# Kernel optimization log

Hardware: AMD Instinct MI355X
Metric: run time of the kernel (lower is better)

## Reference

```python
import jax, jax.numpy as jnp
import numpy as np

N = 4_194_304  # total observations
NBAND = 8      # photometric bands


def setup_inputs() -> dict:
    key = jax.random.key(0)
    ks = jax.random.split(key, 6)
    t = jnp.sort(jax.random.uniform(ks[0], (N,), dtype=jnp.float32) * 10000.0)
    band = jax.random.randint(ks[1], (N,), 0, NBAND)
    y = jax.random.normal(ks[2], (N,), dtype=jnp.float32) * 0.5
    diag = jax.random.uniform(ks[3], (N,), dtype=jnp.float32) * 0.1 + 0.01
    log_amp_delta = jax.random.normal(ks[4], (NBAND - 1,), dtype=jnp.float32) * 0.1
    lag = jax.random.uniform(ks[5], (NBAND - 1,), dtype=jnp.float32) * 5.0
    # exponential (DRW) celerite term: k(tau) = a * exp(-c * tau)
    log_kernel_param = jnp.array([0.0, -3.0], dtype=jnp.float32)
    return {"t": t, "band": band, "y": y, "diag": diag,
            "log_amp_delta": log_amp_delta, "lag": lag,
            "log_kernel_param": log_kernel_param}


def reference(t, band, y, diag, log_amp_delta, lag, log_kernel_param):
    # amp/lag transforms: prepend 0 for the reference band (jnp.insert at 0)
    log_amps = jnp.concatenate([jnp.zeros((1,), log_amp_delta.dtype), log_amp_delta])
    lags = jnp.concatenate([jnp.zeros((1,), lag.dtype), lag])

    # lag-shift times per band, then sort (GP requires sorted inputs)
    new_t = t - lags[band]
    inds = jnp.argsort(new_t)
    ts, bs, ys, ds = new_t[inds], band[inds], y[inds], diag[inds]

    # multiband kernel: K_ij = amp_i * amp_j * a * exp(-c * |t_i - t_j|) + diag_i * delta_ij
    amps = jnp.exp(log_amps)[bs]                 # [N]
    a = jnp.exp(log_kernel_param[0])
    c = jnp.exp(log_kernel_param[1])
    A = ds + a * amps * amps                     # diagonal of K
    U = a * amps                                 # low-rank left factor
    V = amps                                     # low-rank right factor
    dt = jnp.diff(ts, prepend=ts[:1])            # dt[0] = 0
    phi = jnp.exp(-c * dt)                       # transfer factor between neighbors

    # celerite O(N) Cholesky + forward solve (single real term -> scalar state)
    def step(carry, xs):
        Sp, fp = carry                           # Sp = S_{n-1} + D W^2, fp = f_{n-1} + W z
        A_n, U_n, V_n, phi_n, r_n = xs
        S = phi_n * phi_n * Sp
        D = A_n - U_n * U_n * S
        W = (V_n - U_n * S) / D
        f = phi_n * fp
        z = r_n - U_n * f
        return (S + D * W * W, f + W * z), (D, z)

    init = (jnp.zeros((), ys.dtype), jnp.zeros((), ys.dtype))
    _, (D, z) = jax.lax.scan(step, init, (A, U, V, phi, ys))

    n = ys.shape[0]
    log2pi = jnp.log(2 * jnp.pi).astype(ys.dtype)
    logp = -0.5 * (jnp.sum(z * z / D) + jnp.sum(jnp.log(D)) + n * log2pi)
    return -logp  # LCModel.__call__ returns negative log-probability
```

## Files before the change

kernel.cpp:

```cpp
#include <hip/hip_runtime.h>
#include <hip/hip_bf16.h>
#include <math.h>

#define NBAND 8
#define K1_THREADS 1024
#define CHUNK 128
#define HALO  192
#define TILE  16
#define OUTBLK 2048
#define MCAP   3072
#define SEG    32
#define NSEG   128

struct Params {
  float lags[NBAND];
  float amps[NBAND];
  float a, c, kphi1, kphi2;
  int bandstart[NBAND];
  int nb[NBAND];
  int blkbase[NBAND + 1];
};

__device__ __forceinline__ unsigned f2u(float f) {
  unsigned b = __float_as_uint(f);
  return b ^ ((b >> 31) ? 0xFFFFFFFFu : 0x80000000u);
}

__global__ void k1_hist(const int* __restrict__ band, int* __restrict__ cnt) {
  __shared__ int wc[16][NBAND];
  int tid = threadIdx.x;
  int i = blockIdx.x * K1_THREADS + tid;
  int b = band[i];
  int lane = tid & 63, w = tid >> 6;
#pragma unroll
  for (int bb = 0; bb < NBAND; ++bb) {
    unsigned long long m = __ballot(b == bb);
    if (lane == bb) wc[w][bb] = __popcll(m);
  }
  __syncthreads();
  if (tid < NBAND) {
    int s = 0;
#pragma unroll
    for (int w2 = 0; w2 < 16; ++w2) s += wc[w2][tid];
    cnt[blockIdx.x * NBAND + tid] = s;
  }
}

__global__ void k2a_segsum(const int* __restrict__ cnt, int* __restrict__ segsum) {
  int s = blockIdx.x * 256 + threadIdx.x;
  if (s >= NSEG * NBAND) return;
  int b = s & 7, seg = s >> 3;
  int base = seg * SEG;
  int sum = 0;
#pragma unroll 8
  for (int u = 0; u < SEG; ++u) sum += cnt[(base + u) * NBAND + b];
  segsum[s] = sum;
}

__global__ void k2b_scan(const int* __restrict__ segsum, int* __restrict__ segbase,
                         Params* __restrict__ P,
                         const float* __restrict__ lad, const float* __restrict__ lag,
                         const float* __restrict__ lkp, double* __restrict__ acc) {
  __shared__ int sd[NSEG * NBAND];
  __shared__ int tot[NBAND], bstart[NBAND];
  int tid = threadIdx.x;
  if (tid == 0) {
    P->lags[0] = 0.f;
    P->amps[0] = 1.f;
    for (int j = 0; j < NBAND - 1; ++j) {
      P->lags[j + 1] = lag[j];
      P->amps[j + 1] = expf(lad[j]);
    }
    float a = expf(lkp[0]);
    float c = expf(lkp[1]);
    P->a = a;
    P->c = c;
    P->kphi1 = -c * 1.4426950408889634f;
    P->kphi2 = -2.f * c * 1.4426950408889634f;
    acc[0] = 0.0;
    acc[1] = 0.0;
  }
  int b = tid & 7, seg = tid >> 3;
  int sum = segsum[tid];
  int val = sum;
  sd[tid] = val;
  __syncthreads();
  for (int off = 1; off < NSEG; off <<= 1) {
    int yv = (seg >= off) ? sd[tid - off * NBAND] : 0;
    __syncthreads();
    val += yv;
    sd[tid] = val;
    __syncthreads();
  }
  if (seg == NSEG - 1) tot[b] = val;
  __syncthreads();
  if (tid == 0) {
    int g = 0;
    for (int bb = 0; bb < NBAND; ++bb) {
      bstart[bb] = g;
      P->bandstart[bb] = g;
      P->nb[bb] = tot[bb];
      g += tot[bb];
    }
    int s = 0;
    for (int bb = 0; bb < NBAND; ++bb) {
      P->blkbase[bb] = s;
      s += (tot[bb] + 255) / 256;
    }
    P->blkbase[NBAND] = s;
  }
  __syncthreads();
  segbase[tid] = bstart[b] + (val - sum);
}

__global__ void k2c_boff(const int* __restrict__ cnt, const int* __restrict__ segbase,
                         int* __restrict__ boff) {
  int s = blockIdx.x * 256 + threadIdx.x;
  if (s >= NSEG * NBAND) return;
  int b = s & 7, seg = s >> 3;
  int base = seg * SEG;
  int run = segbase[s];
  for (int u = 0; u < SEG; ++u) {
    int idx = (base + u) * NBAND + b;
    int x = cnt[idx];
    boff[idx] = run;
    run += x;
  }
}

__global__ void k3_scatter(const float* __restrict__ t, const int* __restrict__ band,
                           const float* __restrict__ y, const float* __restrict__ dg,
                           const int* __restrict__ boff, const Params* __restrict__ P,
                           float4* __restrict__ payload, float* __restrict__ bt) {
  __shared__ int wc[16][NBAND];
  int tid = threadIdx.x;
  int i = blockIdx.x * K1_THREADS + tid;
  int b = band[i];
  float v = t[i] - P->lags[b];
  int lane = tid & 63, w = tid >> 6;
  int lower = 0;
#pragma unroll
  for (int bb = 0; bb < NBAND; ++bb) {
    unsigned long long m = __ballot(b == bb);
    if (lane == bb) wc[w][bb] = __popcll(m);
    if (b == bb) lower = __popcll(m & ((1ull << lane) - 1ull));
  }
  __syncthreads();
  int base = 0;
  for (int w2 = 0; w2 < w; ++w2) base += wc[w2][b];
  int pos = boff[blockIdx.x * NBAND + b] + base + lower;
  payload[pos] = make_float4(v, y[i], dg[i], P->amps[b]);
  bt[pos] = v;
}

__global__ void k4a_cuts(const float* __restrict__ bt, const Params* __restrict__ P,
                         int* __restrict__ cuts, int nout) {
  int s = blockIdx.x * 64 + threadIdx.x;
  if (s >= (nout + 1) * NBAND) return;
  int oo = s >> 3, b = s & 7;
  int res;
  if (oo == 0) res = 0;
  else if (oo == nout) res = P->nb[b];
  else {
    float vmin = bt[P->bandstart[0]];
    float vmax = bt[P->bandstart[0] + P->nb[0] - 1];
#pragma unroll
    for (int bb = 1; bb < NBAND; ++bb) {
      vmin = fminf(vmin, bt[P->bandstart[bb]]);
      vmax = fmaxf(vmax, bt[P->bandstart[bb] + P->nb[bb] - 1]);
    }
    float v = vmin + (float)((double)(vmax - vmin) * oo / nout);
    unsigned svu = f2u(v);
    const float* p = bt + P->bandstart[b];
    int lo = 0, hi = P->nb[b];
    while (lo < hi) {
      int mid = (lo + hi) >> 1;
      if (f2u(p[mid]) < svu) lo = mid + 1; else hi = mid;
    }
    res = lo;
  }
  cuts[oo * NBAND + b] = res;
}

__global__ __launch_bounds__(256) void k4_merge(const float* __restrict__ bt,
                                                const float4* __restrict__ payload,
                                                const Params* __restrict__ P,
                                                const int* __restrict__ cuts,
                                                float4* __restrict__ out4) {
  __shared__ unsigned long long bufA[MCAP];
  __shared__ unsigned long long bufB[MCAP];
  __shared__ int klo[NBAND], offs[NBAND + 1];
  __shared__ int sbs[NBAND];
  __shared__ long R0s;
  int tid = threadIdx.x;
  int o = blockIdx.x;
  if (tid < NBAND) sbs[tid] = P->bandstart[tid];
  if (tid == 0) {
    int s = 0;
    long r0 = 0;
    for (int b = 0; b < NBAND; ++b) {
      int lo = cuts[o * NBAND + b];
      int hi = cuts[(o + 1) * NBAND + b];
      klo[b] = lo;
      offs[b] = s;
      s += hi - lo;
      r0 += lo;
    }
    offs[NBAND] = s;
    R0s = r0;
  }
  __syncthreads();
  int M = offs[NBAND];
  if (M > MCAP) return;
  int ro[NBAND + 1];
#pragma unroll
  for (int b = 0; b <= NBAND; ++b) ro[b] = offs[b];
  for (int p = tid; p < M; p += 256) {
    int b = 0;
#pragma unroll
    for (int bb = 1; bb < NBAND; ++bb) b += (p >= ro[bb]);
    int w = p - ro[b];
    unsigned u = f2u(bt[sbs[b] + klo[b] + w]);
    bufA[p] = ((unsigned long long)u << 15) | ((unsigned long long)b << 12) | (unsigned)w;
  }
  __syncthreads();
#pragma unroll
  for (int r = 0; r < 3; ++r) {
    const unsigned long long* src = (r == 1) ? bufB : bufA;
    unsigned long long* dst = (r == 1) ? bufA : bufB;
    int h = 1 << r;
    int tpm = 64 << r;
    int mi = tid / tpm, tt = tid % tpm;
    int g = mi * 2 * h;
    int a1 = offs[g], a2 = offs[g + h], a3 = offs[g + 2 * h];
    int n1 = a2 - a1, n2 = a3 - a2;
    int total = n1 + n2;
    int e0 = (int)((long)tt * total / tpm);
    int e1 = (int)((long)(tt + 1) * total / tpm);
    int lo = max(0, e0 - n2), hi = min(e0, n1);
    while (lo < hi) {
      int mid = (lo + hi) >> 1;
      if (src[a1 + mid] < src[a2 + (e0 - mid) - 1]) lo = mid + 1; else hi = mid;
    }
    int i = lo, j = e0 - lo;
    unsigned long long x = (i < n1) ? src[a1 + i] : ~0ull;
    unsigned long long yv = (j < n2) ? src[a2 + j] : ~0ull;
    for (int k = e0; k < e1; ++k) {
      bool tk = x < yv;
      dst[a1 + k] = tk ? x : yv;
      if (tk) { ++i; x = (i < n1) ? src[a1 + i] : ~0ull; }
      else    { ++j; yv = (j < n2) ? src[a2 + j] : ~0ull; }
    }
    __syncthreads();
  }
  long R0 = R0s;
  for (int p = tid; p < M; p += 256) {
    unsigned long long rec = bufB[p];
    int b = (int)((rec >> 12) & 7);
    int w = (int)(rec & 0xFFF);
    out4[R0 + p] = payload[sbs[b] + klo[b] + w];
  }
}

struct ScanState {
  float Sp, fp, tprev, s1, s2;
};

template <bool ACCUM>
__device__ __forceinline__ void step_one(float4 v, ScanState& st, float a, float k1c,
                                         float k2c) {
  float t = v.x, yv = v.y, d = v.z, amp = v.w;
  float dt = t - st.tprev;
  st.tprev = t;
  float e2 = __builtin_amdgcn_exp2f(k2c * dt);
  float e1 = __builtin_amdgcn_exp2f(k1c * dt);
  float U = a * amp;
  float aa2 = U * amp;
  float Aa = d + aa2;
  float c1 = d - aa2;
  float V2 = amp * amp;
  float x = e2 * st.Sp;
  float D = fmaf(-(U * U), x, Aa);
  float r = __builtin_amdgcn_rcpf(D);
  float num = fmaf(c1, x, V2);
  st.Sp = num * r;
  float f = e1 * st.fp;
  float z = fmaf(-U, f, yv);
  float Wn = fmaf(-U, x, amp);
  float W = Wn * r;
  st.fp = fmaf(W, z, f);
  if (ACCUM) {
    st.s1 = fmaf(z * z, r, st.s1);
    st.s2 += __builtin_amdgcn_logf(D);
  }
}

template <bool ACCUM>
__device__ __forceinline__ void run_range(const float4* __restrict__ q, long s, long e,
                                          ScanState& st, float a, float k1c, float k2c) {
  float4 A[TILE], B[TILE];
#pragma unroll
  for (int u = 0; u < TILE; ++u) A[u] = q[s + u];
  for (long tb = s; tb < e; tb += 2 * TILE) {
#pragma unroll
    for (int u = 0; u < TILE; ++u) B[u] = q[tb + TILE + u];
#pragma unroll
    for (int u = 0; u < TILE; ++u) step_one<ACCUM>(A[u], st, a, k1c, k2c);
#pragma unroll
    for (int u = 0; u < TILE; ++u) A[u] = q[tb + 2 * TILE + u];
#pragma unroll
    for (int u = 0; u < TILE; ++u) step_one<ACCUM>(B[u], st, a, k1c, k2c);
  }
}

__global__ __launch_bounds__(64, 1) void k5_scan(const float4* __restrict__ q,
                                                 const Params* __restrict__ P,
                                                 double* __restrict__ acc) {
  int k = blockIdx.x * 64 + threadIdx.x;
  long base = (long)k * CHUNK;
  float a = P->a, k1c = P->kphi1, k2c = P->kphi2;
  ScanState st;
  st.Sp = 0.f;
  st.fp = 0.f;
  st.s1 = 0.f;
  st.s2 = 0.f;
  long s0 = (k == 0) ? base : (base - HALO);
  st.tprev = q[s0].x;
  if (k > 0) run_range<false>(q, base - HALO, base, st, a, k1c, k2c);
  run_range<true>(q, base, base + CHUNK, st, a, k1c, k2c);
  float s1 = st.s1, s2 = st.s2;
#pragma unroll
  for (int off = 32; off > 0; off >>= 1) {
    s1 += __shfl_down(s1, off);
    s2 += __shfl_down(s2, off);
  }
  if (threadIdx.x == 0) {
    atomicAdd(&acc[0], (double)s1);
    atomicAdd(&acc[1], (double)s2);
  }
}

__global__ void k6_final(const double* __restrict__ acc, float* __restrict__ out, long n) {
  double r = 0.5 * (acc[0] + acc[1] * 0.6931471805599453 +
                    (double)n * 1.8378770664093453);
  out[0] = (float)r;
}

extern "C" void kernel_launch(void* const* d_in, const int* in_sizes, int n_in,
                              void* d_out, int out_size, void* d_ws, size_t ws_size,
                              hipStream_t stream) {
  const float* t = (const float*)d_in[0];
  const int* band = (const int*)d_in[1];
  const float* y = (const float*)d_in[2];
  const float* dg = (const float*)d_in[3];
  const float* lad = (const float*)d_in[4];
  const float* lag = (const float*)d_in[5];
  const float* lkp = (const float*)d_in[6];
  float* out = (float*)d_out;
  long N = in_sizes[0];

  char* ws = (char*)d_ws;
  Params* P = (Params*)(ws + 0);
  double* acc = (double*)(ws + 1024);
  int* cnt = (int*)(ws + 8192);
  long nblk = N / K1_THREADS;
  int* boff = (int*)(ws + 8192 + nblk * NBAND * 4);
  int* segsum = (int*)(ws + 270336);
  int* segbase = (int*)(ws + 274432);
  int nout = (int)(N / OUTBLK);
  int* cuts = (int*)(ws + 294912);
  float4* out4 = (float4*)(ws + 524288);
  float4* payload = (float4*)(ws + 524288 + (size_t)N * 16);
  float* bt = (float*)(ws + 524288 + (size_t)N * 32);

  k1_hist<<<(int)nblk, K1_THREADS, 0, stream>>>(band, cnt);
  k2a_segsum<<<(NSEG * NBAND + 255) / 256, 256, 0, stream>>>(cnt, segsum);
  k2b_scan<<<1, NSEG * NBAND, 0, stream>>>(segsum, segbase, P, lad, lag, lkp, acc);
  k2c_boff<<<(NSEG * NBAND + 255) / 256, 256, 0, stream>>>(cnt, segbase, boff);
  k3_scatter<<<(int)nblk, K1_THREADS, 0, stream>>>(t, band, y, dg, boff, P, payload, bt);
  int ncut = ((nout + 1) * NBAND + 63) / 64;
  k4a_cuts<<<ncut, 64, 0, stream>>>(bt, P, cuts, nout);
  k4_merge<<<nout, 256, 0, stream>>>(bt, payload, P, cuts, out4);
  long T = N / CHUNK;
  k5_scan<<<(int)(T / 64), 64, 0, stream>>>(out4, P, acc);
  k6_final<<<1, 1, 0, stream>>>(acc, out, N);
}
```

Baseline: 249.8 us.

## Normalize by band amplitude and pack payload into bf16/fp16 for smaller scan records

Rescales y and diag by the inverse band amplitude so the scan recursion runs with unit amplitudes, then adds the log-amplitude term back in the final reduction. The per-observation payload is packed into 32 bits (bf16 y, fp16 diag) and the merge output shrinks from float4 to float2, with the time recovered from the sort key. This cuts scatter, merge and scan memory traffic roughly in half. The halo and merge shared-memory cap are also reduced, and the atomic accumulation is replaced with per-block partials summed in a 64-thread final kernel. Low-precision y and diag, plus a shorter halo, risk accuracy drift in the log-likelihood.

```diff
diff --git a/kernel.cpp b/kernel.cpp
--- a/kernel.cpp
+++ b/kernel.cpp
@@ -1,20 +1,24 @@
 #include <hip/hip_runtime.h>
 #include <hip/hip_bf16.h>
+#include <hip/hip_fp16.h>
 #include <math.h>
 
 #define NBAND 8
 #define K1_THREADS 1024
 #define CHUNK 128
-#define HALO  192
+#define HALO  128
 #define TILE  16
 #define OUTBLK 2048
-#define MCAP   3072
+#define MCAP   2432
 #define SEG    32
 #define NSEG   128
+#define NPART  512
 
 struct Params {
   float lags[NBAND];
   float amps[NBAND];
+  float inv_amp[NBAND];
+  float inv_amp2[NBAND];
   float a, c, kphi1, kphi2;
   int bandstart[NBAND];
   int nb[NBAND];
@@ -24,6 +28,10 @@
 __device__ __forceinline__ unsigned f2u(float f) {
   unsigned b = __float_as_uint(f);
   return b ^ ((b >> 31) ? 0xFFFFFFFFu : 0x80000000u);
+}
+__device__ __forceinline__ float u2f(unsigned u) {
+  unsigned m = (u & 0x80000000u) ? 0x80000000u : 0xFFFFFFFFu;
+  return __uint_as_float(u ^ m);
 }
 
 __global__ void k1_hist(const int* __restrict__ band, int* __restrict__ cnt) {
@@ -60,16 +68,22 @@
 __global__ void k2b_scan(const int* __restrict__ segsum, int* __restrict__ segbase,
                          Params* __restrict__ P,
                          const float* __restrict__ lad, const float* __restrict__ lag,
-                         const float* __restrict__ lkp, double* __restrict__ acc) {
+                         const float* __restrict__ lkp) {
   __shared__ int sd[NSEG * NBAND];
   __shared__ int tot[NBAND], bstart[NBAND];
   int tid = threadIdx.x;
   if (tid == 0) {
     P->lags[0] = 0.f;
     P->amps[0] = 1.f;
+    P->inv_amp[0] = 1.f;
+    P->inv_amp2[0] = 1.f;
     for (int j = 0; j < NBAND - 1; ++j) {
       P->lags[j + 1] = lag[j];
-      P->amps[j + 1] = expf(lad[j]);
+      float am = expf(lad[j]);
+      P->amps[j + 1] = am;
+      float ia = expf(-lad[j]);
+      P->inv_amp[j + 1] = ia;
+      P->inv_amp2[j + 1] = ia * ia;
     }
     float a = expf(lkp[0]);
     float c = expf(lkp[1]);
@@ -77,8 +91,6 @@
     P->c = c;
     P->kphi1 = -c * 1.4426950408889634f;
     P->kphi2 = -2.f * c * 1.4426950408889634f;
-    acc[0] = 0.0;
-    acc[1] = 0.0;
   }
   int b = tid & 7, seg = tid >> 3;
   int sum = segsum[tid];
@@ -131,7 +143,7 @@
 __global__ void k3_scatter(const float* __restrict__ t, const int* __restrict__ band,
                            const float* __restrict__ y, const float* __restrict__ dg,
                            const int* __restrict__ boff, const Params* __restrict__ P,
-                           float4* __restrict__ payload, float* __restrict__ bt) {
+                           unsigned* __restrict__ pay2, float* __restrict__ bt) {
   __shared__ int wc[16][NBAND];
   int tid = threadIdx.x;
   int i = blockIdx.x * K1_THREADS + tid;
@@ -149,7 +161,12 @@
   int base = 0;
   for (int w2 = 0; w2 < w; ++w2) base += wc[w2][b];
   int pos = boff[blockIdx.x * NBAND + b] + base + lower;
-  payload[pos] = make_float4(v, y[i], dg[i], P->amps[b]);
+  float yp = y[i] * P->inv_amp[b];
+  float dp = dg[i] * P->inv_amp2[b];
+  unsigned yx = __float_as_uint(yp);
+  unsigned yb = (yx + 0x7FFFu + ((yx >> 16) & 1u)) >> 16;
+  unsigned db = (unsigned)__half_as_ushort(__float2half(dp));
+  pay2[pos] = (yb << 16) | db;
   bt[pos] = v;
 }
 
@@ -183,10 +200,10 @@
 }
 
 __global__ __launch_bounds__(256) void k4_merge(const float* __restrict__ bt,
-                                                const float4* __restrict__ payload,
+                                                const unsigned* __restrict__ pay2,
                                                 const Params* __restrict__ P,
                                                 const int* __restrict__ cuts,
-                                                float4* __restrict__ out4) {
+                                                float2* __restrict__ out8) {
   __shared__ unsigned long long bufA[MCAP];
   __shared__ unsigned long long bufB[MCAP];
   __shared__ int klo[NBAND], offs[NBAND + 1];
@@ -258,7 +275,9 @@
     unsigned long long rec = bufB[p];
     int b = (int)((rec >> 12) & 7);
     int w = (int)(rec & 0xFFF);
-    out4[R0 + p] = payload[sbs[b] + klo[b] + w];
+    unsigned key = (unsigned)(rec >> 15);
+    unsigned pv = pay2[sbs[b] + klo[b] + w];
+    out8[R0 + p] = make_float2(u2f(key), __uint_as_float(pv));
   }
 }
 
@@ -267,26 +286,26 @@
 };
 
 template <bool ACCUM>
-__device__ __forceinline__ void step_one(float4 v, ScanState& st, float a, float k1c,
-                                         float k2c) {
-  float t = v.x, yv = v.y, d = v.z, amp = v.w;
+__device__ __forceinline__ void step_one(float2 v, ScanState& st, float a, float a2,
+                                         float k1c, float k2c) {
+  float t = v.x;
+  unsigned pv = __float_as_uint(v.y);
+  float yv = __uint_as_float(pv & 0xFFFF0000u);
+  float d = __half2float(__ushort_as_half((unsigned short)(pv & 0xFFFFu)));
   float dt = t - st.tprev;
   st.tprev = t;
   float e2 = __builtin_amdgcn_exp2f(k2c * dt);
   float e1 = __builtin_amdgcn_exp2f(k1c * dt);
-  float U = a * amp;
-  float aa2 = U * amp;
-  float Aa = d + aa2;
-  float c1 = d - aa2;
-  float V2 = amp * amp;
+  float Aa = d + a;
+  float c1 = d - a;
   float x = e2 * st.Sp;
-  float D = fmaf(-(U * U), x, Aa);
+  float D = fmaf(-a2, x, Aa);
   float r = __builtin_amdgcn_rcpf(D);
-  float num = fmaf(c1, x, V2);
+  float num = fmaf(c1, x, 1.0f);
   st.Sp = num * r;
   float f = e1 * st.fp;
-  float z = fmaf(-U, f, yv);
-  float Wn = fmaf(-U, x, amp);
+  float z = fmaf(-a, f, yv);
+  float Wn = fmaf(-a, x, 1.0f);
   float W = Wn * r;
   st.fp = fmaf(W, z, f);
   if (ACCUM) {
@@ -296,29 +315,30 @@
 }
 
 template <bool ACCUM>
-__device__ __forceinline__ void run_range(const float4* __restrict__ q, long s, long e,
-                                          ScanState& st, float a, float k1c, float k2c) {
-  float4 A[TILE], B[TILE];
+__device__ __forceinline__ void run_range(const float2* __restrict__ q, long s, long e,
+                                          ScanState& st, float a, float a2, float k1c,
+                                          float k2c) {
+  float2 A[TILE], B[TILE];
 #pragma unroll
   for (int u = 0; u < TILE; ++u) A[u] = q[s + u];
   for (long tb = s; tb < e; tb += 2 * TILE) {
 #pragma unroll
     for (int u = 0; u < TILE; ++u) B[u] = q[tb + TILE + u];
 #pragma unroll
-    for (int u = 0; u < TILE; ++u) step_one<ACCUM>(A[u], st, a, k1c, k2c);
+    for (int u = 0; u < TILE; ++u) step_one<ACCUM>(A[u], st, a, a2, k1c, k2c);
 #pragma unroll
     for (int u = 0; u < TILE; ++u) A[u] = q[tb + 2 * TILE + u];
 #pragma unroll
-    for (int u = 0; u < TILE; ++u) step_one<ACCUM>(B[u], st, a, k1c, k2c);
-  }
-}
-
-__global__ __launch_bounds__(64, 1) void k5_scan(const float4* __restrict__ q,
+    for (int u = 0; u < TILE; ++u) step_one<ACCUM>(B[u], st, a, a2, k1c, k2c);
+  }
+}
+
+__global__ __launch_bounds__(64, 1) void k5_scan(const float2* __restrict__ q,
                                                  const Params* __restrict__ P,
-                                                 double* __restrict__ acc) {
+                                                 double2* __restrict__ part) {
   int k = blockIdx.x * 64 + threadIdx.x;
   long base = (long)k * CHUNK;
-  float a = P->a, k1c = P->kphi1, k2c = P->kphi2;
+  float a = P->a, a2 = a * a, k1c = P->kphi1, k2c = P->kphi2;
   ScanState st;
   st.Sp = 0.f;
   st.fp = 0.f;
@@ -326,24 +346,38 @@
   st.s2 = 0.f;
   long s0 = (k == 0) ? base : (base - HALO);
   st.tprev = q[s0].x;
-  if (k > 0) run_range<false>(q, base - HALO, base, st, a, k1c, k2c);
-  run_range<true>(q, base, base + CHUNK, st, a, k1c, k2c);
+  if (k > 0) run_range<false>(q, base - HALO, base, st, a, a2, k1c, k2c);
+  run_range<true>(q, base, base + CHUNK, st, a, a2, k1c, k2c);
   float s1 = st.s1, s2 = st.s2;
 #pragma unroll
   for (int off = 32; off > 0; off >>= 1) {
     s1 += __shfl_down(s1, off);
     s2 += __shfl_down(s2, off);
   }
-  if (threadIdx.x == 0) {
-    atomicAdd(&acc[0], (double)s1);
-    atomicAdd(&acc[1], (double)s2);
-  }
-}
-
-__global__ void k6_final(const double* __restrict__ acc, float* __restrict__ out, long n) {
-  double r = 0.5 * (acc[0] + acc[1] * 0.6931471805599453 +
-                    (double)n * 1.8378770664093453);
-  out[0] = (float)r;
+  if (threadIdx.x == 0) part[blockIdx.x] = make_double2((double)s1, (double)s2);
+}
+
+__global__ void k6_final(const double2* __restrict__ part, const Params* __restrict__ P,
+                         const float* __restrict__ lad, float* __restrict__ out, long n) {
+  int tid = threadIdx.x;
+  double s1 = 0.0, s2 = 0.0;
+  for (int u = tid; u < NPART; u += 64) {
+    double2 p = part[u];
+    s1 += p.x;
+    s2 += p.y;
+  }
+#pragma unroll
+  for (int off = 32; off > 0; off >>= 1) {
+    s1 += __shfl_down(s1, off);
+    s2 += __shfl_down(s2, off);
+  }
+  if (tid == 0) {
+    double ampc = 0.0;
+    for (int b = 1; b < NBAND; ++b) ampc += (double)P->nb[b] * (double)lad[b - 1];
+    double r = 0.5 * (s1 + s2 * 0.6931471805599453 + (double)n * 1.8378770664093453)
+               + ampc;
+    out[0] = (float)r;
+  }
 }
 
 extern "C" void kernel_launch(void* const* d_in, const int* in_sizes, int n_in,
@@ -361,27 +395,27 @@
 
   char* ws = (char*)d_ws;
   Params* P = (Params*)(ws + 0);
-  double* acc = (double*)(ws + 1024);
-  int* cnt = (int*)(ws + 8192);
+  double2* part = (double2*)(ws + 4096);
+  int* cnt = (int*)(ws + 16384);
   long nblk = N / K1_THREADS;
-  int* boff = (int*)(ws + 8192 + nblk * NBAND * 4);
-  int* segsum = (int*)(ws + 270336);
-  int* segbase = (int*)(ws + 274432);
+  int* boff = (int*)(ws + 147456);
+  int* segsum = (int*)(ws + 278528);
+  int* segbase = (int*)(ws + 282624);
   int nout = (int)(N / OUTBLK);
   int* cuts = (int*)(ws + 294912);
-  float4* out4 = (float4*)(ws + 524288);
-  float4* payload = (float4*)(ws + 524288 + (size_t)N * 16);
-  float* bt = (float*)(ws + 524288 + (size_t)N * 32);
+  float2* out8 = (float2*)(ws + 524288);
+  unsigned* pay2 = (unsigned*)(ws + 524288 + (size_t)N * 8);
+  float* bt = (float*)(ws + 524288 + (size_t)N * 12);
 
   k1_hist<<<(int)nblk, K1_THREADS, 0, stream>>>(band, cnt);
   k2a_segsum<<<(NSEG * NBAND + 255) / 256, 256, 0, stream>>>(cnt, segsum);
-  k2b_scan<<<1, NSEG * NBAND, 0, stream>>>(segsum, segbase, P, lad, lag, lkp, acc);
+  k2b_scan<<<1, NSEG * NBAND, 0, stream>>>(segsum, segbase, P, lad, lag, lkp);
   k2c_boff<<<(NSEG * NBAND + 255) / 256, 256, 0, stream>>>(cnt, segbase, boff);
-  k3_scatter<<<(int)nblk, K1_THREADS, 0, stream>>>(t, band, y, dg, boff, P, payload, bt);
+  k3_scatter<<<(int)nblk, K1_THREADS, 0, stream>>>(t, band, y, dg, boff, P, pay2, bt);
   int ncut = ((nout + 1) * NBAND + 63) / 64;
   k4a_cuts<<<ncut, 64, 0, stream>>>(bt, P, cuts, nout);
-  k4_merge<<<nout, 256, 0, stream>>>(bt, payload, P, cuts, out4);
+  k4_merge<<<nout, 256, 0, stream>>>(bt, pay2, P, cuts, out8);
   long T = N / CHUNK;
-  k5_scan<<<(int)(T / 64), 64, 0, stream>>>(out4, P, acc);
-  k6_final<<<1, 1, 0, stream>>>(acc, out, N);
-}
+  k5_scan<<<(int)(T / 64), 64, 0, stream>>>(out8, P, part);
+  k6_final<<<1, 64, 0, stream>>>(part, P, lad, out, N);
+}
```

Result: faster. 201.3 us (-19.4%).
